# Kernel optimization log

Hardware: AMD Instinct MI355X
Metric: run time of the kernel (lower is better)

The kernel has to match this reference:

```python
import jax, jax.numpy as jnp
import numpy as np

KERNEL_SIZE = 5
NUM_BUCKETS = 25


def setup_inputs() -> dict:
    key = jax.random.key(0)
    k1, k2, k3 = jax.random.split(key, 3)
    B, C, H, W = 8, 96, 192, 192
    inp = jax.random.normal(k1, (B, C, H, W), dtype=jnp.float32)
    kernel_bank = jax.random.normal(k2, (NUM_BUCKETS, KERNEL_SIZE, KERNEL_SIZE), dtype=jnp.float32)
    buckets = jax.random.randint(k3, (B, H, W), 0, NUM_BUCKETS, dtype=jnp.int64)
    return {"input": inp, "kernel_bank": kernel_bank, "buckets": buckets}


def reference(input, kernel_bank, buckets):
    # Per-pixel kernel selection from a bank, applied depthwise (same kernel for
    # every channel at a given spatial location), with 'same' zero padding.
    K = KERNEL_SIZE
    p = (K - 1) // 2
    B, C, H, W = input.shape
    xpad = jnp.pad(input, ((0, 0), (0, 0), (p, p), (p, p)))  # [B,C,H+K-1,W+K-1]
    kb = kernel_bank[buckets]  # [B,H,W,K,K] gathered per-pixel kernels
    out = jnp.zeros_like(input)
    # Fixed small loop over the K*K kernel taps (unrolled by jit); avoids
    # materializing a [B,C,H,W,K,K] patch tensor.
    for i in range(K):
        for j in range(K):
            out = out + xpad[:, :, i:i + H, j:j + W] * kb[:, None, :, :, i, j]
    return out
```

## Files before the change

kernel.cpp:

```cpp
#include <hip/hip_runtime.h>


#define KS 5
#define NB 25
#define HALO 2
#define TH 8
#define RPT 4
#define WID 192
#define HEI 192
#define CH 96
#define NBATCH 8
#define LPAD 4
#define LROW (LPAD + WID + LPAD)
#define LH (TH + 2 * HALO)
#define CSPLIT 4
#define CPB (CH / CSPLIT)
#define NTHREADS (WID * (TH / RPT))
#define HW ((size_t)HEI * WID)

static_assert(CPB % 2 == 0, "channel loop processes channel pairs");

__device__ __forceinline__ void async16(void* lds, const void* g) {
    __builtin_amdgcn_global_load_lds(
        (const __attribute__((address_space(1))) void*)g,
        (__attribute__((address_space(3))) void*)lds, 16, 0, 0);
}

#define WDECL(R)                                                              \
    float w##R##_0, w##R##_1, w##R##_2, w##R##_3, w##R##_4, w##R##_5,         \
        w##R##_6, w##R##_7, w##R##_8, w##R##_9, w##R##_10, w##R##_11,         \
        w##R##_12, w##R##_13, w##R##_14, w##R##_15, w##R##_16, w##R##_17,     \
        w##R##_18, w##R##_19, w##R##_20, w##R##_21, w##R##_22, w##R##_23,     \
        w##R##_24;

#define WGATH(R)                                                              \
    {                                                                         \
        const float* wp = &sb[bkt##R * (KS * KS)];                            \
        w##R##_0 = wp[0];   w##R##_1 = wp[1];   w##R##_2 = wp[2];             \
        w##R##_3 = wp[3];   w##R##_4 = wp[4];   w##R##_5 = wp[5];             \
        w##R##_6 = wp[6];   w##R##_7 = wp[7];   w##R##_8 = wp[8];             \
        w##R##_9 = wp[9];   w##R##_10 = wp[10]; w##R##_11 = wp[11];           \
        w##R##_12 = wp[12]; w##R##_13 = wp[13]; w##R##_14 = wp[14];           \
        w##R##_15 = wp[15]; w##R##_16 = wp[16]; w##R##_17 = wp[17];           \
        w##R##_18 = wp[18]; w##R##_19 = wp[19]; w##R##_20 = wp[20];           \
        w##R##_21 = wp[21]; w##R##_22 = wp[22]; w##R##_23 = wp[23];           \
        w##R##_24 = wp[24];                                                   \
    }

#define F5(R, T0, T1, T2, T3, T4)                                             \
    acc##R += x0 * w##R##_##T0 + x1 * w##R##_##T1 + x2 * w##R##_##T2          \
            + x3 * w##R##_##T3 + x4 * w##R##_##T4;

#define K0(R) F5(R, 0, 1, 2, 3, 4)
#define K1(R) F5(R, 5, 6, 7, 8, 9)
#define K2(R) F5(R, 10, 11, 12, 13, 14)
#define K3(R) F5(R, 15, 16, 17, 18, 19)
#define K4(R) F5(R, 20, 21, 22, 23, 24)

#define LOADX(CUR, SLAB, I)                                                   \
    {                                                                         \
        const float* rp = &sin_[CUR][SLAB][ty4 + (I)][wcol + (LPAD - HALO)];  \
        x0 = rp[0]; x1 = rp[1]; x2 = rp[2]; x3 = rp[3]; x4 = rp[4];           \
    }

__global__ __launch_bounds__(NTHREADS, 3) void csconv_kernel(
    const float* __restrict__ in, const float* __restrict__ bank,
    const int* __restrict__ buckets, float* __restrict__ out)
{
    __shared__ float sb[NB * KS * KS];
    __shared__ __align__(16) float sin_[2][2][LH][LROW];

    const int tid  = threadIdx.x;
    const int wcol = tid % WID;
    const int ty   = tid / WID;
    const int lane = tid & 63;
    const int wv   = tid >> 6;
    const int cg   = blockIdx.x;
    const int ht   = blockIdx.y;
    const int b    = blockIdx.z;
    const int h0   = ht * TH;
    const int r0   = h0 + ty * RPT;

    const int c0 = cg * CPB;
    const float* inb  = in  + (size_t)(b * CH + c0) * HW;
    float*       outb = out + (size_t)(b * CH + c0) * HW;

    for (int t = tid; t < NB * KS * KS; t += NTHREADS) sb[t] = bank[t];

    {
        const int s = tid / 96, rem = tid % 96;
        const int r = rem / 8, p = rem % 8;
        const int col = (p < 4) ? p : (WID + p);
        sin_[s >> 1][s & 1][r][col] = 0.0f;
    }
    if (h0 - HALO < 0) {
        for (int t = tid; t < 4 * 2 * LROW; t += NTHREADS) {
            const int s = t / (2 * LROW), rem = t % (2 * LROW);
            sin_[s >> 1][s & 1][rem / LROW][rem % LROW] = 0.0f;
        }
    }
    if (h0 + TH + HALO > HEI) {
        for (int t = tid; t < 4 * 2 * LROW; t += NTHREADS) {
            const int s = t / (2 * LROW), rem = t % (2 * LROW);
            sin_[s >> 1][s & 1][LH - 2 + rem / LROW][rem % LROW] = 0.0f;
        }
    }

#pragma unroll
    for (int s = 0; s < 2; ++s)
#pragma unroll
        for (int k = 0; k < 2; ++k) {
            const int rr = 2 * wv + k;
            const int hg = h0 - HALO + rr;
            if (hg >= 0 && hg < HEI && lane < 48)
                async16(&sin_[0][s][rr][LPAD],
                        inb + (size_t)s * HW + (size_t)hg * WID + lane * 4);
        }

    __syncthreads();

    const int bkt0 = buckets[(b * HEI + r0 + 0) * WID + wcol];
    const int bkt1 = buckets[(b * HEI + r0 + 1) * WID + wcol];
    const int bkt2 = buckets[(b * HEI + r0 + 2) * WID + wcol];
    const int bkt3 = buckets[(b * HEI + r0 + 3) * WID + wcol];
    WDECL(0) WDECL(1) WDECL(2) WDECL(3)
    WGATH(0) WGATH(1) WGATH(2) WGATH(3)

    const int ty4 = ty * RPT;

#define CONV_STORE(CUR, SLAB, CIDX)                                           \
    {                                                                         \
        float acc0 = 0.0f, acc1 = 0.0f, acc2 = 0.0f, acc3 = 0.0f;             \
        float x0, x1, x2, x3, x4;                                             \
        LOADX(CUR, SLAB, 0) K0(0)                                             \
        LOADX(CUR, SLAB, 1) K1(0) K0(1)                                       \
        LOADX(CUR, SLAB, 2) K2(0) K1(1) K0(2)                                 \
        LOADX(CUR, SLAB, 3) K3(0) K2(1) K1(2) K0(3)                           \
        LOADX(CUR, SLAB, 4) K4(0) K3(1) K2(2) K1(3)                           \
        LOADX(CUR, SLAB, 5) K4(1) K3(2) K2(3)                                 \
        LOADX(CUR, SLAB, 6) K4(2) K3(3)                                       \
        LOADX(CUR, SLAB, 7) K4(3)                                             \
        float* op = outb + (size_t)(CIDX) * HW + (size_t)r0 * WID + wcol;     \
        op[0 * WID] = acc0; op[1 * WID] = acc1;                               \
        op[2 * WID] = acc2; op[3 * WID] = acc3;                               \
    }

    for (int c = 0; c < CPB; c += 2) {
        const int cur = (c >> 1) & 1;
        const bool has_next = (c + 2 < CPB);

        if (has_next) {
            const int nxt = cur ^ 1;
#pragma unroll
            for (int s = 0; s < 2; ++s)
#pragma unroll
                for (int k = 0; k < 2; ++k) {
                    const int rr = 2 * wv + k;
                    const int hg = h0 - HALO + rr;
                    if (hg >= 0 && hg < HEI && lane < 48)
                        async16(&sin_[nxt][s][rr][LPAD],
                                inb + (size_t)(c + 2 + s) * HW
                                    + (size_t)hg * WID + lane * 4);
                }
        }

        CONV_STORE(cur, 0, c)
        CONV_STORE(cur, 1, c + 1)

        if (has_next) {
            asm volatile("s_waitcnt vmcnt(8)" ::: "memory");
            __builtin_amdgcn_s_barrier();
            asm volatile("" ::: "memory");
        }
    }
}

extern "C" void kernel_launch(void* const* d_in, const int* in_sizes, int n_in,
                              void* d_out, int out_size, void* d_ws, size_t ws_size,
                              hipStream_t stream) {
    const float* in      = (const float*)d_in[0];
    const float* bank    = (const float*)d_in[1];
    const int*   buckets = (const int*)d_in[2];
    float*       out     = (float*)d_out;
    dim3 grid(CSPLIT, HEI / TH, NBATCH);
    csconv_kernel<<<grid, NTHREADS, 0, stream>>>(in, bank, buckets, out);
}
```

Measured before the change: 226.9 us.

## Halve rows per thread to double block size and cut register pressure

Each thread now computes 2 output rows instead of 4, so a block has 768 threads (12 waves) instead of 384. Per-thread weight registers drop from 100 to 50, and the async LDS staging is redistributed so each wave loads two rows spread across both channel slabs. The waitcnt, launch bounds and init guards are adjusted to match. The trade-off is less vertical reuse of LDS rows per thread, giving more LDS reads per output, in exchange for more waves in flight.

```diff
diff --git a/kernel.cpp b/kernel.cpp
--- a/kernel.cpp
+++ b/kernel.cpp
@@ -5,7 +5,7 @@
 #define NB 25
 #define HALO 2
 #define TH 8
-#define RPT 4
+#define RPT 2
 #define WID 192
 #define HEI 192
 #define CH 96
@@ -16,9 +16,11 @@
 #define CSPLIT 4
 #define CPB (CH / CSPLIT)
 #define NTHREADS (WID * (TH / RPT))
+#define NWAVES (NTHREADS / 64)
 #define HW ((size_t)HEI * WID)
 
 static_assert(CPB % 2 == 0, "channel loop processes channel pairs");
+static_assert(NTHREADS <= 1024, "block size limit");
 
 __device__ __forceinline__ void async16(void* lds, const void* g) {
     __builtin_amdgcn_global_load_lds(
@@ -59,11 +61,11 @@
 
 #define LOADX(CUR, SLAB, I)                                                   \
     {                                                                         \
-        const float* rp = &sin_[CUR][SLAB][ty4 + (I)][wcol + (LPAD - HALO)];  \
+        const float* rp = &sin_[CUR][SLAB][ty2 + (I)][wcol + (LPAD - HALO)];  \
         x0 = rp[0]; x1 = rp[1]; x2 = rp[2]; x3 = rp[3]; x4 = rp[4];           \
     }
 
-__global__ __launch_bounds__(NTHREADS, 3) void csconv_kernel(
+__global__ __launch_bounds__(NTHREADS, 2) void csconv_kernel(
     const float* __restrict__ in, const float* __restrict__ bank,
     const int* __restrict__ buckets, float* __restrict__ out)
 {
@@ -85,9 +87,9 @@
     const float* inb  = in  + (size_t)(b * CH + c0) * HW;
     float*       outb = out + (size_t)(b * CH + c0) * HW;
 
-    for (int t = tid; t < NB * KS * KS; t += NTHREADS) sb[t] = bank[t];
+    if (tid < NB * KS * KS) sb[tid] = bank[tid];
 
-    {
+    if (tid < 4 * LH * 8) {
         const int s = tid / 96, rem = tid % 96;
         const int r = rem / 8, p = rem % 8;
         const int col = (p < 4) ? p : (WID + p);
@@ -107,42 +109,37 @@
     }
 
 #pragma unroll
-    for (int s = 0; s < 2; ++s)
-#pragma unroll
-        for (int k = 0; k < 2; ++k) {
-            const int rr = 2 * wv + k;
-            const int hg = h0 - HALO + rr;
-            if (hg >= 0 && hg < HEI && lane < 48)
-                async16(&sin_[0][s][rr][LPAD],
-                        inb + (size_t)s * HW + (size_t)hg * WID + lane * 4);
-        }
+    for (int k = 0; k < 2; ++k) {
+        const int m  = 2 * wv + k;
+        const int s  = m / LH;
+        const int rr = m % LH;
+        const int hg = h0 - HALO + rr;
+        if (hg >= 0 && hg < HEI && lane < 48)
+            async16(&sin_[0][s][rr][LPAD],
+                    inb + (size_t)s * HW + (size_t)hg * WID + lane * 4);
+    }
 
     __syncthreads();
 
     const int bkt0 = buckets[(b * HEI + r0 + 0) * WID + wcol];
     const int bkt1 = buckets[(b * HEI + r0 + 1) * WID + wcol];
-    const int bkt2 = buckets[(b * HEI + r0 + 2) * WID + wcol];
-    const int bkt3 = buckets[(b * HEI + r0 + 3) * WID + wcol];
-    WDECL(0) WDECL(1) WDECL(2) WDECL(3)
-    WGATH(0) WGATH(1) WGATH(2) WGATH(3)
+    WDECL(0) WDECL(1)
+    WGATH(0) WGATH(1)
 
-    const int ty4 = ty * RPT;
+    const int ty2 = ty * RPT;
 
 #define CONV_STORE(CUR, SLAB, CIDX)                                           \
     {                                                                         \
-        float acc0 = 0.0f, acc1 = 0.0f, acc2 = 0.0f, acc3 = 0.0f;             \
+        float acc0 = 0.0f, acc1 = 0.0f;                                       \
         float x0, x1, x2, x3, x4;                                             \
         LOADX(CUR, SLAB, 0) K0(0)                                             \
         LOADX(CUR, SLAB, 1) K1(0) K0(1)                                       \
-        LOADX(CUR, SLAB, 2) K2(0) K1(1) K0(2)                                 \
-        LOADX(CUR, SLAB, 3) K3(0) K2(1) K1(2) K0(3)                           \
-        LOADX(CUR, SLAB, 4) K4(0) K3(1) K2(2) K1(3)                           \
-        LOADX(CUR, SLAB, 5) K4(1) K3(2) K2(3)                                 \
-        LOADX(CUR, SLAB, 6) K4(2) K3(3)                                       \
-        LOADX(CUR, SLAB, 7) K4(3)                                             \
+        LOADX(CUR, SLAB, 2) K2(0) K1(1)                                       \
+        LOADX(CUR, SLAB, 3) K3(0) K2(1)                                       \
+        LOADX(CUR, SLAB, 4) K4(0) K3(1)                                       \
+        LOADX(CUR, SLAB, 5) K4(1)                                             \
         float* op = outb + (size_t)(CIDX) * HW + (size_t)r0 * WID + wcol;     \
         op[0 * WID] = acc0; op[1 * WID] = acc1;                               \
-        op[2 * WID] = acc2; op[3 * WID] = acc3;                               \
     }
 
     for (int c = 0; c < CPB; c += 2) {
@@ -152,23 +149,23 @@
         if (has_next) {
             const int nxt = cur ^ 1;
 #pragma unroll
-            for (int s = 0; s < 2; ++s)
-#pragma unroll
-                for (int k = 0; k < 2; ++k) {
-                    const int rr = 2 * wv + k;
-                    const int hg = h0 - HALO + rr;
-                    if (hg >= 0 && hg < HEI && lane < 48)
-                        async16(&sin_[nxt][s][rr][LPAD],
-                                inb + (size_t)(c + 2 + s) * HW
-                                    + (size_t)hg * WID + lane * 4);
-                }
+            for (int k = 0; k < 2; ++k) {
+                const int m  = 2 * wv + k;
+                const int s  = m / LH;
+                const int rr = m % LH;
+                const int hg = h0 - HALO + rr;
+                if (hg >= 0 && hg < HEI && lane < 48)
+                    async16(&sin_[nxt][s][rr][LPAD],
+                            inb + (size_t)(c + 2 + s) * HW
+                                + (size_t)hg * WID + lane * 4);
+            }
         }
 
         CONV_STORE(cur, 0, c)
         CONV_STORE(cur, 1, c + 1)
 
         if (has_next) {
-            asm volatile("s_waitcnt vmcnt(8)" ::: "memory");
+            asm volatile("s_waitcnt vmcnt(4)" ::: "memory");
             __builtin_amdgcn_s_barrier();
             asm volatile("" ::: "memory");
         }
```

After: 211.2 us. 6.9% less time.
